# Optimization experiments

Measured on AMD Instinct MI355X. Metric: run time of the kernel, lower is better.

## Reference

```python
import jax, jax.numpy as jnp
import numpy as np

BN_EPS = 1e-5

def setup_inputs() -> dict:
    key = jax.random.key(0)
    k1, k2, k3 = jax.random.split(key, 3)
    B, N, C, K, O = 4, 16384, 64, 16, 64
    x = jax.random.normal(k1, (B, N, C), dtype=jnp.float32)
    idx = jax.random.randint(k2, (B, N, K), 0, N, dtype=jnp.int32)
    weight = jax.random.normal(k3, (O, 2 * C), dtype=jnp.float32) * 0.05
    gamma = jnp.ones((O,), dtype=jnp.float32)
    beta = jnp.zeros((O,), dtype=jnp.float32)
    return {"x": x, "idx": idx, "weight": weight, "gamma": gamma, "beta": beta}

def reference(x, idx, weight, gamma, beta):
    # x: [B,N,C], idx: [B,N,k] kNN indices into N
    B, N, C = x.shape
    k = idx.shape[2]
    # irregular gather: neighbor features [B,N,k,C]
    batch_ix = jnp.arange(B)[:, None, None]
    neighbor = x[batch_ix, idx]                     # [B,N,k,C]
    center = x[:, :, None, :]                       # [B,N,1,C]
    diff = neighbor - center                        # [B,N,k,C]
    edge = jnp.concatenate([jnp.broadcast_to(center, (B, N, k, C)), diff], axis=-1)  # [B,N,k,2C]
    # 1x1 conv == per-edge linear transform: [B,N,k,O]
    h = jnp.einsum('bnkc,oc->bnko', edge, weight)
    # BatchNorm2d in training mode: stats over (B,N,k) per output channel
    mean = jnp.mean(h, axis=(0, 1, 2))
    var = jnp.var(h, axis=(0, 1, 2))
    h = (h - mean) * jax.lax.rsqrt(var + BN_EPS) * gamma + beta
    h = jax.nn.relu(h)
    # max-pool over k neighbors -> [B,N,O]
    out = jnp.max(h, axis=2)
    return out
```

## Files before the change

kernel.cpp:

```cpp
#include <hip/hip_runtime.h>
#include <hip/hip_fp16.h>
#include <math.h>

#define BN_EPS 1e-5f

constexpr int B_ = 4, N_ = 16384, C_ = 64, K_ = 16, O_ = 64;
constexpr int ROWS = B_ * N_;
constexpr int RPB_A = 128;
constexpr int NBLK_A = ROWS / RPB_A;
constexpr int RPB_B = 64;
constexpr int NBLK_B = ROWS / RPB_B;

typedef float  vf4 __attribute__((ext_vector_type(4)));
typedef int    vi4 __attribute__((ext_vector_type(4)));

__device__ __forceinline__ float4 nt_load4(const float* p) {
    vf4 v = __builtin_nontemporal_load((const vf4*)p);
    return make_float4(v.x, v.y, v.z, v.w);
}
__device__ __forceinline__ void nt_store4(float* p, float4 v) {
    vf4 t; t.x = v.x; t.y = v.y; t.z = v.z; t.w = v.w;
    __builtin_nontemporal_store(t, (vf4*)p);
}

struct __align__(8) H4 { __half2 a, b; };

__device__ __forceinline__ float4 h4_to_f4(H4 h) {
    const float2 p01 = __half22float2(h.a);
    const float2 p23 = __half22float2(h.b);
    return make_float4(p01.x, p01.y, p23.x, p23.y);
}
__device__ __forceinline__ H4 f4_to_h4(float4 v) {
    H4 h;
    h.a = __floats2half2_rn(v.x, v.y);
    h.b = __floats2half2_rn(v.z, v.w);
    return h;
}

__global__ __launch_bounds__(256) void pass_a(const float* __restrict__ x,
                                              const float* __restrict__ w,
                                              __half* __restrict__ y1h,
                                              __half* __restrict__ y2h) {
    __shared__ __align__(16) float xs[64 * 132];
    __shared__ __align__(16) float w1m[64 * 64];
    __shared__ __align__(16) float w2s[64 * 64];
    const int tid = threadIdx.x;

    const int blk = blockIdx.x;
    const int xcd = blk & 7;
    const int bt = xcd >> 1;
    const int slot = ((blk >> 3) << 1) | (xcd & 1);
    const long base = (long)bt * N_ + (long)slot * RPB_A;

    for (int i = tid; i < 64 * 16; i += 256) {
        const int o = i & 63;
        const int c4 = i >> 6;
        const float4 wa = *(const float4*)&w[o * 128 + c4 * 4];
        const float4 wb = *(const float4*)&w[o * 128 + 64 + c4 * 4];
        w1m[(c4 * 4 + 0) * 64 + o] = wa.x - wb.x;
        w1m[(c4 * 4 + 1) * 64 + o] = wa.y - wb.y;
        w1m[(c4 * 4 + 2) * 64 + o] = wa.z - wb.z;
        w1m[(c4 * 4 + 3) * 64 + o] = wa.w - wb.w;
        w2s[(c4 * 4 + 0) * 64 + o] = wb.x;
        w2s[(c4 * 4 + 1) * 64 + o] = wb.y;
        w2s[(c4 * 4 + 2) * 64 + o] = wb.z;
        w2s[(c4 * 4 + 3) * 64 + o] = wb.w;
    }

    const float* xsrc = x + base * 64;
    for (int i = tid; i < RPB_A * 16; i += 256) {
        const int row = i >> 4;
        const int c4 = i & 15;
        const float4 v = nt_load4(xsrc + i * 4);
        xs[(c4 * 4 + 0) * 132 + row] = v.x;
        xs[(c4 * 4 + 1) * 132 + row] = v.y;
        xs[(c4 * 4 + 2) * 132 + row] = v.z;
        xs[(c4 * 4 + 3) * 132 + row] = v.w;
    }
    __syncthreads();

    const int o0 = (tid & 15) * 4;
    const int r0 = (tid >> 4) * 8;
    float a1[8][4] = {{0.f}};
    float a2[8][4] = {{0.f}};

#pragma unroll 4
    for (int c = 0; c < 64; ++c) {
        const float4 xv0 = *(const float4*)&xs[c * 132 + r0];
        const float4 xv1 = *(const float4*)&xs[c * 132 + r0 + 4];
        const float4 w1v = *(const float4*)&w1m[c * 64 + o0];
        const float4 w2v = *(const float4*)&w2s[c * 64 + o0];
        const float xr[8] = {xv0.x, xv0.y, xv0.z, xv0.w,
                             xv1.x, xv1.y, xv1.z, xv1.w};
#pragma unroll
        for (int r = 0; r < 8; ++r) {
            a1[r][0] = fmaf(xr[r], w1v.x, a1[r][0]);
            a1[r][1] = fmaf(xr[r], w1v.y, a1[r][1]);
            a1[r][2] = fmaf(xr[r], w1v.z, a1[r][2]);
            a1[r][3] = fmaf(xr[r], w1v.w, a1[r][3]);
            a2[r][0] = fmaf(xr[r], w2v.x, a2[r][0]);
            a2[r][1] = fmaf(xr[r], w2v.y, a2[r][1]);
            a2[r][2] = fmaf(xr[r], w2v.z, a2[r][2]);
            a2[r][3] = fmaf(xr[r], w2v.w, a2[r][3]);
        }
    }

#pragma unroll
    for (int r = 0; r < 8; ++r) {
        *(H4*)(y1h + (base + r0 + r) * 64 + o0) =
            f4_to_h4(make_float4(a1[r][0], a1[r][1], a1[r][2], a1[r][3]));
        *(H4*)(y2h + (base + r0 + r) * 64 + o0) =
            f4_to_h4(make_float4(a2[r][0], a2[r][1], a2[r][2], a2[r][3]));
    }
}

__global__ __launch_bounds__(256) void pass_b(const __half* __restrict__ y1h,
                                              const __half* __restrict__ y2h,
                                              const int* __restrict__ idx,
                                              const float* __restrict__ gamma,
                                              __half* __restrict__ exth,
                                              float* __restrict__ partial) {
    __shared__ int sidx[RPB_B * K_];
    __shared__ float reds[4][64];
    __shared__ float redq[4][64];
    const int tid = threadIdx.x;
    const int blk = blockIdx.x;
    const int xcd = blk & 7;
    const int bt = xcd >> 1;
    const int slot = ((blk >> 3) << 1) | (xcd & 1);
    const long base = (long)bt * N_ + (long)slot * RPB_B;

    {
        vi4 iv = __builtin_nontemporal_load(
            (const vi4*)(idx + base * K_) + tid);
        ((vi4*)sidx)[tid] = iv;
    }

    const int lane = tid & 63;
    const int wv   = tid >> 6;
    const int ksub = lane >> 4;
    const int c4   = lane & 15;
    const __half* y2b = y2h + (long)bt * N_ * 64;

    const float4 gm = ((const float4*)gamma)[c4];
    const float4 sgn = make_float4(gm.x >= 0.f ? 1.f : -1.f,
                                   gm.y >= 0.f ? 1.f : -1.f,
                                   gm.z >= 0.f ? 1.f : -1.f,
                                   gm.w >= 0.f ? 1.f : -1.f);
    __syncthreads();

    float4 psum = make_float4(0.f, 0.f, 0.f, 0.f);
    float4 psq  = make_float4(0.f, 0.f, 0.f, 0.f);

    for (int rl = wv; rl < RPB_B; rl += 8) {
        const long rowA = base + rl;
        const long rowB = base + rl + 4;
        H4 gA[4], gB[4];
#pragma unroll
        for (int kk = 0; kk < 4; ++kk) {
            const int m = sidx[rl * K_ + kk * 4 + ksub];
            gA[kk] = *(const H4*)(y2b + (long)m * 64 + c4 * 4);
        }
#pragma unroll
        for (int kk = 0; kk < 4; ++kk) {
            const int m = sidx[(rl + 4) * K_ + kk * 4 + ksub];
            gB[kk] = *(const H4*)(y2b + (long)m * 64 + c4 * 4);
        }
        const float4 y1A = h4_to_f4(*(const H4*)(y1h + rowA * 64 + c4 * 4));
        const float4 y1B = h4_to_f4(*(const H4*)(y1h + rowB * 64 + c4 * 4));

        float4 eA = make_float4(-3.402823466e+38f, -3.402823466e+38f,
                                -3.402823466e+38f, -3.402823466e+38f);
        float4 eB = eA;
#pragma unroll
        for (int kk = 0; kk < 4; ++kk) {
            const float2 f01 = __half22float2(gA[kk].a);
            const float2 f23 = __half22float2(gA[kk].b);
            const float hx = y1A.x + f01.x, hy = y1A.y + f01.y;
            const float hz = y1A.z + f23.x, hw = y1A.w + f23.y;
            eA.x = fmaxf(eA.x, sgn.x * hx); eA.y = fmaxf(eA.y, sgn.y * hy);
            eA.z = fmaxf(eA.z, sgn.z * hz); eA.w = fmaxf(eA.w, sgn.w * hw);
            psum.x += hx; psum.y += hy; psum.z += hz; psum.w += hw;
            psq.x = fmaf(hx, hx, psq.x); psq.y = fmaf(hy, hy, psq.y);
            psq.z = fmaf(hz, hz, psq.z); psq.w = fmaf(hw, hw, psq.w);
        }
#pragma unroll
        for (int kk = 0; kk < 4; ++kk) {
            const float2 f01 = __half22float2(gB[kk].a);
            const float2 f23 = __half22float2(gB[kk].b);
            const float hx = y1B.x + f01.x, hy = y1B.y + f01.y;
            const float hz = y1B.z + f23.x, hw = y1B.w + f23.y;
            eB.x = fmaxf(eB.x, sgn.x * hx); eB.y = fmaxf(eB.y, sgn.y * hy);
            eB.z = fmaxf(eB.z, sgn.z * hz); eB.w = fmaxf(eB.w, sgn.w * hw);
            psum.x += hx; psum.y += hy; psum.z += hz; psum.w += hw;
            psq.x = fmaf(hx, hx, psq.x); psq.y = fmaf(hy, hy, psq.y);
            psq.z = fmaf(hz, hz, psq.z); psq.w = fmaf(hw, hw, psq.w);
        }
#pragma unroll
        for (int d = 16; d <= 32; d <<= 1) {
            eA.x = fmaxf(eA.x, __shfl_xor(eA.x, d));
            eA.y = fmaxf(eA.y, __shfl_xor(eA.y, d));
            eA.z = fmaxf(eA.z, __shfl_xor(eA.z, d));
            eA.w = fmaxf(eA.w, __shfl_xor(eA.w, d));
            eB.x = fmaxf(eB.x, __shfl_xor(eB.x, d));
            eB.y = fmaxf(eB.y, __shfl_xor(eB.y, d));
            eB.z = fmaxf(eB.z, __shfl_xor(eB.z, d));
            eB.w = fmaxf(eB.w, __shfl_xor(eB.w, d));
        }
        if (ksub == 0) {
            *(H4*)(exth + rowA * 64 + c4 * 4) =
                f4_to_h4(make_float4(sgn.x * eA.x, sgn.y * eA.y,
                                     sgn.z * eA.z, sgn.w * eA.w));
            *(H4*)(exth + rowB * 64 + c4 * 4) =
                f4_to_h4(make_float4(sgn.x * eB.x, sgn.y * eB.y,
                                     sgn.z * eB.z, sgn.w * eB.w));
        }
    }
#pragma unroll
    for (int d = 16; d <= 32; d <<= 1) {
        psum.x += __shfl_xor(psum.x, d); psum.y += __shfl_xor(psum.y, d);
        psum.z += __shfl_xor(psum.z, d); psum.w += __shfl_xor(psum.w, d);
        psq.x  += __shfl_xor(psq.x, d);  psq.y  += __shfl_xor(psq.y, d);
        psq.z  += __shfl_xor(psq.z, d);  psq.w  += __shfl_xor(psq.w, d);
    }
    if (ksub == 0) {
        *(float4*)&reds[wv][c4 * 4] = psum;
        *(float4*)&redq[wv][c4 * 4] = psq;
    }
    __syncthreads();
    if (tid < 64) {
        const float s = reds[0][tid] + reds[1][tid] + reds[2][tid] + reds[3][tid];
        const float q = redq[0][tid] + redq[1][tid] + redq[2][tid] + redq[3][tid];
        partial[blk * 128 + tid] = s;
        partial[blk * 128 + 64 + tid] = q;
    }
}

__global__ __launch_bounds__(256) void pass_c(const float* __restrict__ partial,
                                              const float* __restrict__ gamma,
                                              const float* __restrict__ beta,
                                              float* __restrict__ ss) {
    __shared__ double rs[256];
    __shared__ double rq[256];
    const int o = blockIdx.x;
    const int tid = threadIdx.x;
    double as = 0.0, aq = 0.0;
    for (int i = tid; i < NBLK_B; i += 256) {
        as += (double)partial[i * 128 + o];
        aq += (double)partial[i * 128 + 64 + o];
    }
    rs[tid] = as;
    rq[tid] = aq;
    __syncthreads();
    for (int s = 128; s > 0; s >>= 1) {
        if (tid < s) { rs[tid] += rs[tid + s]; rq[tid] += rq[tid + s]; }
        __syncthreads();
    }
    if (tid == 0) {
        const double cnt = (double)B_ * N_ * K_;
        double mean = rs[0] / cnt;
        double var = rq[0] / cnt - mean * mean;
        float scale = gamma[o] * (float)(1.0 / sqrt(var + (double)BN_EPS));
        float shift = beta[o] - (float)mean * scale;
        ss[o] = scale;
        ss[64 + o] = shift;
    }
}

__global__ __launch_bounds__(256) void pass_d(const __half* __restrict__ exth,
                                              const float* __restrict__ ss,
                                              float* __restrict__ out) {
    __shared__ float sscale[64], sshift[64];
    const int tid = threadIdx.x;
    if (tid < 64) { sscale[tid] = ss[tid]; sshift[tid] = ss[64 + tid]; }
    __syncthreads();
    const long total4 = (long)ROWS * 64 / 4;
    for (long i = (long)blockIdx.x * 256 + tid; i < total4;
         i += (long)gridDim.x * 256) {
        const int c0 = ((int)i * 4) & 63;
        const float4 e = h4_to_f4(*(const H4*)(exth + i * 4));
        float4 r;
        r.x = fmaxf(fmaf(sscale[c0],     e.x, sshift[c0]),     0.f);
        r.y = fmaxf(fmaf(sscale[c0 + 1], e.y, sshift[c0 + 1]), 0.f);
        r.z = fmaxf(fmaf(sscale[c0 + 2], e.z, sshift[c0 + 2]), 0.f);
        r.w = fmaxf(fmaf(sscale[c0 + 3], e.w, sshift[c0 + 3]), 0.f);
        nt_store4(out + i * 4, r);
    }
}

extern "C" void kernel_launch(void* const* d_in, const int* in_sizes, int n_in,
                              void* d_out, int out_size, void* d_ws, size_t ws_size,
                              hipStream_t stream) {
    const float* x     = (const float*)d_in[0];
    const int*   idx   = (const int*)d_in[1];
    const float* w     = (const float*)d_in[2];
    const float* gamma = (const float*)d_in[3];
    const float* beta  = (const float*)d_in[4];
    float* out = (float*)d_out;

    float* ws = (float*)d_ws;
    __half* y1h     = (__half*)ws;
    __half* y2h     = (__half*)(ws + (long)ROWS * 32);
    __half* exth    = (__half*)(ws + (long)ROWS * 64);
    float*  partial = ws + (long)ROWS * 96;
    float*  ss      = partial + (long)NBLK_B * 128;

    pass_a<<<NBLK_A, 256, 0, stream>>>(x, w, y1h, y2h);
    pass_b<<<NBLK_B, 256, 0, stream>>>(y1h, y2h, idx, gamma, exth, partial);
    pass_c<<<64, 256, 0, stream>>>(partial, gamma, beta, ss);
    pass_d<<<2048, 256, 0, stream>>>(exth, ss, out);
}
```

Measured before the change: 120.7 us.

## Use fp16 MFMA with swizzled LDS tiles for the pass_a linear transform

Replaces the fp32 scalar FMA register-blocked GEMM in pass_a with 16x16x32 fp16 MFMA instructions. x and the combined (W1-W2, W2) weight matrix are converted to fp16 and stored in LDS with an XOR swizzle to avoid bank conflicts. The goal is to cut the compute cost of pass_a and halve its LDS footprint. Inputs are now quantized to fp16 before the matmul, which lowers accuracy. The output is written as scattered 2-byte stores per lane, which may coalesce poorly.

```diff
diff --git a/kernel.cpp b/kernel.cpp
--- a/kernel.cpp
+++ b/kernel.cpp
@@ -11,8 +11,11 @@
 constexpr int RPB_B = 64;
 constexpr int NBLK_B = ROWS / RPB_B;
 
-typedef float  vf4 __attribute__((ext_vector_type(4)));
-typedef int    vi4 __attribute__((ext_vector_type(4)));
+typedef float    vf4   __attribute__((ext_vector_type(4)));
+typedef int      vi4   __attribute__((ext_vector_type(4)));
+typedef _Float16 f16x4 __attribute__((ext_vector_type(4)));
+typedef _Float16 f16x8 __attribute__((ext_vector_type(8)));
+typedef float    f32x4 __attribute__((ext_vector_type(4)));
 
 __device__ __forceinline__ float4 nt_load4(const float* p) {
     vf4 v = __builtin_nontemporal_load((const vf4*)p);
@@ -41,77 +44,99 @@
                                               const float* __restrict__ w,
                                               __half* __restrict__ y1h,
                                               __half* __restrict__ y2h) {
-    __shared__ __align__(16) float xs[64 * 132];
-    __shared__ __align__(16) float w1m[64 * 64];
-    __shared__ __align__(16) float w2s[64 * 64];
+    __shared__ __align__(16) _Float16 xs[128 * 64];
+    __shared__ __align__(16) _Float16 wsh[128 * 64];
     const int tid = threadIdx.x;
 
     const int blk = blockIdx.x;
     const int xcd = blk & 7;
     const int bt = xcd >> 1;
-    const int slot = ((blk >> 3) << 1) | (xcd & 1);
-    const long base = (long)bt * N_ + (long)slot * RPB_A;
-
-    for (int i = tid; i < 64 * 16; i += 256) {
-        const int o = i & 63;
-        const int c4 = i >> 6;
-        const float4 wa = *(const float4*)&w[o * 128 + c4 * 4];
-        const float4 wb = *(const float4*)&w[o * 128 + 64 + c4 * 4];
-        w1m[(c4 * 4 + 0) * 64 + o] = wa.x - wb.x;
-        w1m[(c4 * 4 + 1) * 64 + o] = wa.y - wb.y;
-        w1m[(c4 * 4 + 2) * 64 + o] = wa.z - wb.z;
-        w1m[(c4 * 4 + 3) * 64 + o] = wa.w - wb.w;
-        w2s[(c4 * 4 + 0) * 64 + o] = wb.x;
-        w2s[(c4 * 4 + 1) * 64 + o] = wb.y;
-        w2s[(c4 * 4 + 2) * 64 + o] = wb.z;
-        w2s[(c4 * 4 + 3) * 64 + o] = wb.w;
+    const int slot_b = ((blk >> 3) << 1) | (xcd & 1);
+    const long base = (long)bt * N_ + (long)slot_b * RPB_A;
+
+    for (int i = tid; i < 128 * 16; i += 256) {
+        const int o = i >> 4;
+        const int c4 = i & 15;
+        float4 v;
+        if (o < 64) {
+            const float4 wa = *(const float4*)&w[o * 128 + c4 * 4];
+            const float4 wb = *(const float4*)&w[o * 128 + 64 + c4 * 4];
+            v = make_float4(wa.x - wb.x, wa.y - wb.y, wa.z - wb.z, wa.w - wb.w);
+        } else {
+            v = *(const float4*)&w[(o - 64) * 128 + 64 + c4 * 4];
+        }
+        const int addr = o * 64 + (((c4 >> 1) ^ (o & 7)) << 3) + ((c4 & 1) << 2);
+        f16x4 hv;
+        hv[0] = (_Float16)v.x; hv[1] = (_Float16)v.y;
+        hv[2] = (_Float16)v.z; hv[3] = (_Float16)v.w;
+        *(f16x4*)&wsh[addr] = hv;
     }
 
     const float* xsrc = x + base * 64;
-    for (int i = tid; i < RPB_A * 16; i += 256) {
+    for (int i = tid; i < 128 * 16; i += 256) {
         const int row = i >> 4;
         const int c4 = i & 15;
         const float4 v = nt_load4(xsrc + i * 4);
-        xs[(c4 * 4 + 0) * 132 + row] = v.x;
-        xs[(c4 * 4 + 1) * 132 + row] = v.y;
-        xs[(c4 * 4 + 2) * 132 + row] = v.z;
-        xs[(c4 * 4 + 3) * 132 + row] = v.w;
-    }
-    __syncthreads();
-
-    const int o0 = (tid & 15) * 4;
-    const int r0 = (tid >> 4) * 8;
-    float a1[8][4] = {{0.f}};
-    float a2[8][4] = {{0.f}};
-
-#pragma unroll 4
-    for (int c = 0; c < 64; ++c) {
-        const float4 xv0 = *(const float4*)&xs[c * 132 + r0];
-        const float4 xv1 = *(const float4*)&xs[c * 132 + r0 + 4];
-        const float4 w1v = *(const float4*)&w1m[c * 64 + o0];
-        const float4 w2v = *(const float4*)&w2s[c * 64 + o0];
-        const float xr[8] = {xv0.x, xv0.y, xv0.z, xv0.w,
-                             xv1.x, xv1.y, xv1.z, xv1.w};
-#pragma unroll
-        for (int r = 0; r < 8; ++r) {
-            a1[r][0] = fmaf(xr[r], w1v.x, a1[r][0]);
-            a1[r][1] = fmaf(xr[r], w1v.y, a1[r][1]);
-            a1[r][2] = fmaf(xr[r], w1v.z, a1[r][2]);
-            a1[r][3] = fmaf(xr[r], w1v.w, a1[r][3]);
-            a2[r][0] = fmaf(xr[r], w2v.x, a2[r][0]);
-            a2[r][1] = fmaf(xr[r], w2v.y, a2[r][1]);
-            a2[r][2] = fmaf(xr[r], w2v.z, a2[r][2]);
-            a2[r][3] = fmaf(xr[r], w2v.w, a2[r][3]);
-        }
-    }
-
-#pragma unroll
-    for (int r = 0; r < 8; ++r) {
-        *(H4*)(y1h + (base + r0 + r) * 64 + o0) =
-            f4_to_h4(make_float4(a1[r][0], a1[r][1], a1[r][2], a1[r][3]));
-        *(H4*)(y2h + (base + r0 + r) * 64 + o0) =
-            f4_to_h4(make_float4(a2[r][0], a2[r][1], a2[r][2], a2[r][3]));
-    }
+        const int addr = row * 64 + (((c4 >> 1) ^ (row & 7)) << 3) + ((c4 & 1) << 2);
+        f16x4 hv;
+        hv[0] = (_Float16)v.x; hv[1] = (_Float16)v.y;
+        hv[2] = (_Float16)v.z; hv[3] = (_Float16)v.w;
+        *(f16x4*)&xs[addr] = hv;
+    }
+    __syncthreads();
+
+    const int wv   = tid >> 6;
+    const int lane = tid & 63;
+    const int lrow = lane & 15;
+    const int lk   = lane >> 4;
+    const int r0   = wv * 32;
+
+    f32x4 acc[2][8];
+#pragma unroll
+    for (int i = 0; i < 2; ++i)
+#pragma unroll
+        for (int j = 0; j < 8; ++j)
+            acc[i][j] = (f32x4){0.f, 0.f, 0.f, 0.f};
+
+    f16x8 af[2][2];
+#pragma unroll
+    for (int rf = 0; rf < 2; ++rf)
+#pragma unroll
+        for (int kk = 0; kk < 2; ++kk) {
+            const int row = r0 + rf * 16 + lrow;
+            const int slot = kk * 4 + lk;
+            af[rf][kk] = *(const f16x8*)&xs[row * 64 + ((slot ^ (row & 7)) << 3)];
+        }
+
+#pragma unroll
+    for (int cf = 0; cf < 8; ++cf) {
+#pragma unroll
+        for (int kk = 0; kk < 2; ++kk) {
+            const int o = cf * 16 + lrow;
+            const int slot = kk * 4 + lk;
+            const f16x8 bfr =
+                *(const f16x8*)&wsh[o * 64 + ((slot ^ (o & 7)) << 3)];
+            acc[0][cf] = __builtin_amdgcn_mfma_f32_16x16x32_f16(
+                af[0][kk], bfr, acc[0][cf], 0, 0, 0);
+            acc[1][cf] = __builtin_amdgcn_mfma_f32_16x16x32_f16(
+                af[1][kk], bfr, acc[1][cf], 0, 0, 0);
+        }
+    }
+
+#pragma unroll
+    for (int rf = 0; rf < 2; ++rf)
+#pragma unroll
+        for (int cf = 0; cf < 8; ++cf) {
+            const int col = cf * 16 + lrow;
+            __half* dst = (col < 64)
+                ? (y1h + (long)col)
+                : (y2h + (long)(col - 64));
+#pragma unroll
+            for (int r = 0; r < 4; ++r) {
+                const long row = base + r0 + rf * 16 + lk * 4 + r;
+                dst[row * 64] = __float2half(acc[rf][cf][r]);
+            }
+        }
 }
 
 __global__ __launch_bounds__(256) void pass_b(const __half* __restrict__ y1h,
```

Result: faster. 113.2 us (-6.3%).
